# Kernel optimization log

Measured on AMD Instinct MI355X. Metric: run time of the kernel, lower is better.

Reference implementation:

```python
import jax, jax.numpy as jnp
import numpy as np

LN_EPS = 1e-5

def layer_norm(x, w, b):
    mu = jnp.mean(x, axis=-1, keepdims=True)
    var = jnp.mean(jnp.square(x - mu), axis=-1, keepdims=True)
    return (x - mu) * jax.lax.rsqrt(var + LN_EPS) * w + b

def setup_inputs() -> dict:
    key = jax.random.key(0)
    ks = jax.random.split(key, 8)
    B, F, Q, D = 8, 4096, 64, 1024
    H, DH = 16, 64
    inner = H * DH
    s = 1.0 / np.sqrt(D)
    return {
        "features": jax.random.normal(ks[0], (B, F, D), jnp.float32),
        "latents": jax.random.normal(ks[1], (B, Q, D), jnp.float32),
        "key_attention_mask": jax.random.randint(ks[2], (B, F), 0, 2, jnp.int32),
        "ln_m_w": jnp.ones((D,), jnp.float32),
        "ln_m_b": jnp.zeros((D,), jnp.float32),
        "ln_l_w": jnp.ones((D,), jnp.float32),
        "ln_l_b": jnp.zeros((D,), jnp.float32),
        "Wq": jax.random.normal(ks[3], (D, inner), jnp.float32) * s,
        "Wk": jax.random.normal(ks[4], (D, inner), jnp.float32) * s,
        "Wv": jax.random.normal(ks[5], (D, inner), jnp.float32) * s,
        "Wo": jax.random.normal(ks[6], (inner, D), jnp.float32) * (1.0 / np.sqrt(inner)),
    }

def reference(features, latents, key_attention_mask, ln_m_w, ln_m_b, ln_l_w, ln_l_b, Wq, Wk, Wv, Wo):
    H, DH = 16, 64
    B, F, D = features.shape
    Q = latents.shape[1]
    scale = DH ** (-0.5)

    x = layer_norm(features, ln_m_w, ln_m_b)          # [B,F,D]
    lat = layer_norm(latents, ln_l_w, ln_l_b)          # [B,Q,D]

    q = (lat @ Wq).reshape(B, Q, H, DH).transpose(0, 2, 1, 3)   # [B,H,Q,DH]
    kv_in = jnp.concatenate([x, lat], axis=1)                    # [B,F+Q,D]
    k = (kv_in @ Wk).reshape(B, F + Q, H, DH).transpose(0, 2, 1, 3)
    v = (kv_in @ Wv).reshape(B, F + Q, H, DH).transpose(0, 2, 1, 3)

    q = q * scale
    sim = jnp.einsum('bhqd,bhfd->bhqf', q, k)                    # [B,H,Q,F+Q]

    full_mask = jnp.concatenate(
        [key_attention_mask, jnp.ones((B, Q), key_attention_mask.dtype)], axis=1)  # [B,F+Q]
    sim = jnp.where(full_mask[:, None, None, :] == 0, -jnp.inf, sim)

    sim = sim - jax.lax.stop_gradient(jnp.max(sim, axis=-1, keepdims=True))
    alphas = jax.nn.softmax(sim, axis=-1)
    out = jnp.einsum('bhqf,bhfv->bhqv', alphas, v)               # [B,H,Q,DH]
    out = out.transpose(0, 2, 1, 3).reshape(B, Q, H * DH)        # [B,Q,inner]
    return out @ Wo                                              # [B,Q,D]
```

## Files before the change

kernel.cpp:

```cpp
#include <hip/hip_runtime.h>
#include <hip/hip_bf16.h>

#define B_    8
#define F_    4096
#define Qn    64
#define Dm    1024
#define Hh    16
#define DHn   64
#define FQ    4160
#define ROWS_KV 33280
#define ROWS_F  32768
#define KS    13
#define CHPB  5
#define KVOFF ((size_t)ROWS_KV * 1024)

typedef __bf16 v8bf __attribute__((ext_vector_type(8)));
typedef __bf16 v4bf __attribute__((ext_vector_type(4)));
typedef float  v4f  __attribute__((ext_vector_type(4)));

__device__ inline void gl_lds16(const __bf16* g, __bf16* l) {
  __builtin_amdgcn_global_load_lds((__attribute__((address_space(1))) void*)(g),
                                   (__attribute__((address_space(3))) void*)(l),
                                   16, 0, 0);
}

__device__ inline bool is_bf16_inputs(const void* mw) {
  return ((const unsigned int*)mw)[0] != 0x3F800000u;
}

__global__ __launch_bounds__(256) void transpose_kernel(
    const void* __restrict__ w0, const void* __restrict__ w1,
    const void* __restrict__ w2, const void* __restrict__ w3,
    __bf16* __restrict__ t0, __bf16* __restrict__ t1,
    __bf16* __restrict__ t2, __bf16* __restrict__ t3,
    const void* __restrict__ mw)
{
  bool bf = is_bf16_inputs(mw);
  __shared__ __bf16 tile[32][33];
  const void* src; __bf16* dst;
  switch (blockIdx.z) {
    case 0: src = w0; dst = t0; break;
    case 1: src = w1; dst = t1; break;
    case 2: src = w2; dst = t2; break;
    default: src = w3; dst = t3; break;
  }
  int tx = threadIdx.x, ty = threadIdx.y;
  int x = blockIdx.x * 32 + tx;
  #pragma unroll
  for (int j = 0; j < 4; ++j) {
    int y = blockIdx.y * 32 + ty + j * 8;
    size_t e = (size_t)y * 1024 + x;
    float v = bf ? (float)((const __bf16*)src)[e] : ((const float*)src)[e];
    tile[ty + j * 8][tx] = (__bf16)v;
  }
  __syncthreads();
  int x2 = blockIdx.y * 32 + tx;
  #pragma unroll
  for (int j = 0; j < 4; ++j) {
    int y2 = blockIdx.x * 32 + ty + j * 8;
    dst[(size_t)y2 * 1024 + x2] = tile[tx][ty + j * 8];
  }
}

__global__ __launch_bounds__(256) void ln_kernel(
    const void* __restrict__ feat, const void* __restrict__ lat,
    const void* __restrict__ mw, const void* __restrict__ mb,
    const void* __restrict__ lw, const void* __restrict__ lb,
    __bf16* __restrict__ kv_bf, __bf16* __restrict__ lat_bf)
{
  bool bf = is_bf16_inputs(mw);
  int tid = threadIdx.x;
  int wave = tid >> 6, lane = tid & 63;
  int r = blockIdx.x * 4 + wave;
  const void *rowp, *w, *g;
  __bf16 *dst, *dst2 = nullptr;
  size_t rowoff;
  if (r < ROWS_F) {
    rowoff = (size_t)r * Dm; rowp = feat; w = mw; g = mb;
    int b = r >> 12, f = r & (F_ - 1);
    dst = kv_bf + ((size_t)b * FQ + f) * Dm;
  } else {
    int r2 = r - ROWS_F;
    rowoff = (size_t)r2 * Dm; rowp = lat; w = lw; g = lb;
    int b = r2 >> 6, q = r2 & 63;
    dst  = kv_bf + ((size_t)b * FQ + F_ + q) * Dm;
    dst2 = lat_bf + (size_t)r2 * Dm;
  }
  float xs[16], ws_[16], gs[16];
  if (bf) {
    const __bf16* rp = (const __bf16*)rowp + rowoff;
    const __bf16* wp = (const __bf16*)w;
    const __bf16* gp = (const __bf16*)g;
    #pragma unroll
    for (int g2 = 0; g2 < 2; ++g2) {
      int base = g2 * 512 + lane * 8;
      v8bf X = *(const v8bf*)(rp + base);
      v8bf W = *(const v8bf*)(wp + base);
      v8bf G = *(const v8bf*)(gp + base);
      #pragma unroll
      for (int j = 0; j < 8; ++j) {
        xs[g2*8+j] = (float)X[j]; ws_[g2*8+j] = (float)W[j]; gs[g2*8+j] = (float)G[j];
      }
    }
  } else {
    const float* rp = (const float*)rowp + rowoff;
    const float* wp = (const float*)w;
    const float* gp = (const float*)g;
    #pragma unroll
    for (int g4 = 0; g4 < 4; ++g4) {
      int base = g4 * 256 + lane * 4;
      float4 X = *(const float4*)(rp + base);
      float4 W = *(const float4*)(wp + base);
      float4 G = *(const float4*)(gp + base);
      xs[g4*4]=X.x; xs[g4*4+1]=X.y; xs[g4*4+2]=X.z; xs[g4*4+3]=X.w;
      ws_[g4*4]=W.x; ws_[g4*4+1]=W.y; ws_[g4*4+2]=W.z; ws_[g4*4+3]=W.w;
      gs[g4*4]=G.x; gs[g4*4+1]=G.y; gs[g4*4+2]=G.z; gs[g4*4+3]=G.w;
    }
  }
  float s = 0.f, ss = 0.f;
  #pragma unroll
  for (int j = 0; j < 16; ++j) { s += xs[j]; ss += xs[j] * xs[j]; }
  #pragma unroll
  for (int off = 32; off > 0; off >>= 1) {
    s  += __shfl_xor(s, off, 64);
    ss += __shfl_xor(ss, off, 64);
  }
  float mean = s * (1.f / 1024.f);
  float var  = ss * (1.f / 1024.f) - mean * mean;
  float rs = rsqrtf(var + 1e-5f);
  float os[16];
  #pragma unroll
  for (int j = 0; j < 16; ++j) os[j] = (xs[j] - mean) * rs * ws_[j] + gs[j];
  if (bf) {
    #pragma unroll
    for (int g2 = 0; g2 < 2; ++g2) {
      int base = g2 * 512 + lane * 8;
      v8bf O;
      #pragma unroll
      for (int j = 0; j < 8; ++j) O[j] = (__bf16)os[g2*8+j];
      *(v8bf*)(dst + base) = O;
      if (dst2) *(v8bf*)(dst2 + base) = O;
    }
  } else {
    #pragma unroll
    for (int g4 = 0; g4 < 4; ++g4) {
      int base = g4 * 256 + lane * 4;
      v4bf O;
      #pragma unroll
      for (int j = 0; j < 4; ++j) O[j] = (__bf16)os[g4*4+j];
      *(v4bf*)(dst + base) = O;
      if (dst2) *(v4bf*)(dst2 + base) = O;
    }
  }
}

__global__ __launch_bounds__(256, 2) void gemm_kv2_kernel(
    const __bf16* __restrict__ A, const __bf16* __restrict__ BtKV,
    __bf16* __restrict__ KVb)
{
  __shared__ __align__(16) __bf16 As0[128 * 32];
  __shared__ __align__(16) __bf16 As1[128 * 32];
  __shared__ __align__(16) __bf16 Bk0[128 * 32];
  __shared__ __align__(16) __bf16 Bk1[128 * 32];
  __shared__ __align__(16) __bf16 Bv0[128 * 32];
  __shared__ __align__(16) __bf16 Bv1[128 * 32];
  int tid = threadIdx.x;
  int lane = tid & 63, wave = tid >> 6;
  int wm = wave >> 1, wn = wave & 1;
  int n0 = blockIdx.x * 128, m0 = blockIdx.y * 128;
  int lm = lane & 15, lk = (lane >> 4) << 3;

  v4f ak[4][4], av[4][4];
  #pragma unroll
  for (int i = 0; i < 4; ++i)
    #pragma unroll
    for (int j = 0; j < 4; ++j) {
      ak[i][j] = (v4f){0.f, 0.f, 0.f, 0.f};
      av[i][j] = (v4f){0.f, 0.f, 0.f, 0.f};
    }

  int c0 = tid, c1 = tid + 256;
  const __bf16* a0p = A    + (size_t)(m0 + (c0 >> 2)) * 1024 + ((c0 & 3) << 3);
  const __bf16* a1p = A    + (size_t)(m0 + (c1 >> 2)) * 1024 + ((c1 & 3) << 3);
  const __bf16* b0p = BtKV + (size_t)(n0 + (c0 >> 2)) * 1024 + ((c0 & 3) << 3);
  const __bf16* b1p = BtKV + (size_t)(n0 + (c1 >> 2)) * 1024 + ((c1 & 3) << 3);
  const size_t VW = (size_t)1024 * 1024;

  for (int k0 = 0; k0 < 1024; k0 += 64) {
    __syncthreads();
    gl_lds16(a0p + k0,           &As0[c0 * 8]);
    gl_lds16(a1p + k0,           &As0[c1 * 8]);
    gl_lds16(a0p + k0 + 32,      &As1[c0 * 8]);
    gl_lds16(a1p + k0 + 32,      &As1[c1 * 8]);
    gl_lds16(b0p + k0,           &Bk0[c0 * 8]);
    gl_lds16(b1p + k0,           &Bk0[c1 * 8]);
    gl_lds16(b0p + k0 + 32,      &Bk1[c0 * 8]);
    gl_lds16(b1p + k0 + 32,      &Bk1[c1 * 8]);
    gl_lds16(b0p + VW + k0,      &Bv0[c0 * 8]);
    gl_lds16(b1p + VW + k0,      &Bv0[c1 * 8]);
    gl_lds16(b0p + VW + k0 + 32, &Bv1[c0 * 8]);
    gl_lds16(b1p + VW + k0 + 32, &Bv1[c1 * 8]);
    __syncthreads();
    {
      v8bf a[4], bk[4], bv[4];
      #pragma unroll
      for (int i = 0; i < 4; ++i) a[i]  = *(const v8bf*)&As0[(wm * 64 + i * 16 + lm) * 32 + lk];
      #pragma unroll
      for (int j = 0; j < 4; ++j) bk[j] = *(const v8bf*)&Bk0[(wn * 64 + j * 16 + lm) * 32 + lk];
      #pragma unroll
      for (int j = 0; j < 4; ++j) bv[j] = *(const v8bf*)&Bv0[(wn * 64 + j * 16 + lm) * 32 + lk];
      #pragma unroll
      for (int i = 0; i < 4; ++i)
        #pragma unroll
        for (int j = 0; j < 4; ++j) {
          ak[i][j] = __builtin_amdgcn_mfma_f32_16x16x32_bf16(a[i], bk[j], ak[i][j], 0, 0, 0);
          av[i][j] = __builtin_amdgcn_mfma_f32_16x16x32_bf16(a[i], bv[j], av[i][j], 0, 0, 0);
        }
    }
    {
      v8bf a[4], bk[4], bv[4];
      #pragma unroll
      for (int i = 0; i < 4; ++i) a[i]  = *(const v8bf*)&As1[(wm * 64 + i * 16 + lm) * 32 + lk];
      #pragma unroll
      for (int j = 0; j < 4; ++j) bk[j] = *(const v8bf*)&Bk1[(wn * 64 + j * 16 + lm) * 32 + lk];
      #pragma unroll
      for (int j = 0; j < 4; ++j) bv[j] = *(const v8bf*)&Bv1[(wn * 64 + j * 16 + lm) * 32 + lk];
      #pragma unroll
      for (int i = 0; i < 4; ++i)
        #pragma unroll
        for (int j = 0; j < 4; ++j) {
          ak[i][j] = __builtin_amdgcn_mfma_f32_16x16x32_bf16(a[i], bk[j], ak[i][j], 0, 0, 0);
          av[i][j] = __builtin_amdgcn_mfma_f32_16x16x32_bf16(a[i], bv[j], av[i][j], 0, 0, 0);
        }
    }
  }

  #pragma unroll
  for (int i = 0; i < 4; ++i)
    #pragma unroll
    for (int j = 0; j < 4; ++j) {
      int col = n0 + wn * 64 + j * 16 + lm;
      #pragma unroll
      for (int reg = 0; reg < 4; ++reg) {
        int row = m0 + wm * 64 + i * 16 + (lane >> 4) * 4 + reg;
        int bb = row / FQ; int f = row - bb * FQ;
        size_t idx = ((size_t)(bb * Hh + (col >> 6)) * FQ + f) * 64 + (col & 63);
        KVb[idx]         = (__bf16)ak[i][j][reg];
        KVb[idx + KVOFF] = (__bf16)av[i][j][reg];
      }
    }
}

__global__ __launch_bounds__(256) void gemm2_kernel(
    const __bf16* __restrict__ A, const __bf16* __restrict__ Bt,
    void* __restrict__ C, int mode, int out_follow,
    const void* __restrict__ mw)
{
  int obf = out_follow ? (is_bf16_inputs(mw) ? 1 : 0) : 1;

  __shared__ __align__(16) __bf16 As0[128 * 32];
  __shared__ __align__(16) __bf16 As1[128 * 32];
  __shared__ __align__(16) __bf16 Bs0[128 * 32];
  __shared__ __align__(16) __bf16 Bs1[128 * 32];
  int tid = threadIdx.x;
  int lane = tid & 63, wave = tid >> 6;
  int wm = wave >> 1, wn = wave & 1;
  int m0 = blockIdx.y * 128, n0 = blockIdx.x * 128;
  int lm = lane & 15, lk = (lane >> 4) << 3;

  v4f acc[4][4];
  #pragma unroll
  for (int i = 0; i < 4; ++i)
    #pragma unroll
    for (int j = 0; j < 4; ++j) acc[i][j] = (v4f){0.f, 0.f, 0.f, 0.f};

  int c0 = tid, c1 = tid + 256;
  const __bf16* a0p = A  + (size_t)(m0 + (c0 >> 2)) * 1024 + ((c0 & 3) << 3);
  const __bf16* a1p = A  + (size_t)(m0 + (c1 >> 2)) * 1024 + ((c1 & 3) << 3);
  const __bf16* b0p = Bt + (size_t)(n0 + (c0 >> 2)) * 1024 + ((c0 & 3) << 3);
  const __bf16* b1p = Bt + (size_t)(n0 + (c1 >> 2)) * 1024 + ((c1 & 3) << 3);

  for (int k0 = 0; k0 < 1024; k0 += 64) {
    __syncthreads();
    gl_lds16(a0p + k0,      &As0[c0 * 8]);
    gl_lds16(a1p + k0,      &As0[c1 * 8]);
    gl_lds16(a0p + k0 + 32, &As1[c0 * 8]);
    gl_lds16(a1p + k0 + 32, &As1[c1 * 8]);
    gl_lds16(b0p + k0,      &Bs0[c0 * 8]);
    gl_lds16(b1p + k0,      &Bs0[c1 * 8]);
    gl_lds16(b0p + k0 + 32, &Bs1[c0 * 8]);
    gl_lds16(b1p + k0 + 32, &Bs1[c1 * 8]);
    __syncthreads();
    {
      v8bf a[4], b[4];
      #pragma unroll
      for (int i = 0; i < 4; ++i) a[i] = *(const v8bf*)&As0[(wm * 64 + i * 16 + lm) * 32 + lk];
      #pragma unroll
      for (int j = 0; j < 4; ++j) b[j] = *(const v8bf*)&Bs0[(wn * 64 + j * 16 + lm) * 32 + lk];
      #pragma unroll
      for (int i = 0; i < 4; ++i)
        #pragma unroll
        for (int j = 0; j < 4; ++j)
          acc[i][j] = __builtin_amdgcn_mfma_f32_16x16x32_bf16(a[i], b[j], acc[i][j], 0, 0, 0);
    }
    {
      v8bf a[4], b[4];
      #pragma unroll
      for (int i = 0; i < 4; ++i) a[i] = *(const v8bf*)&As1[(wm * 64 + i * 16 + lm) * 32 + lk];
      #pragma unroll
      for (int j = 0; j < 4; ++j) b[j] = *(const v8bf*)&Bs1[(wn * 64 + j * 16 + lm) * 32 + lk];
      #pragma unroll
      for (int i = 0; i < 4; ++i)
        #pragma unroll
        for (int j = 0; j < 4; ++j)
          acc[i][j] = __builtin_amdgcn_mfma_f32_16x16x32_bf16(a[i], b[j], acc[i][j], 0, 0, 0);
    }
  }

  #pragma unroll
  for (int i = 0; i < 4; ++i)
    #pragma unroll
    for (int j = 0; j < 4; ++j) {
      int col = n0 + wn * 64 + j * 16 + lm;
      #pragma unroll
      for (int reg = 0; reg < 4; ++reg) {
        int row = m0 + wm * 64 + i * 16 + (lane >> 4) * 4 + reg;
        size_t idx;
        if (mode == 0) {
          idx = (size_t)row * 1024 + col;
        } else {
          int bb = row >> 6; int qq = row & 63;
          idx = ((size_t)(bb * Hh + (col >> 6)) * 64 + qq) * 64 + (col & 63);
        }
        float v = acc[i][j][reg];
        if (obf) ((__bf16*)C)[idx] = (__bf16)v;
        else     ((float*)C)[idx]  = v;
      }
    }
}

__global__ __launch_bounds__(256) void attn_part_kernel(
    const __bf16* __restrict__ Qm, const __bf16* __restrict__ K,
    const __bf16* __restrict__ V, const int* __restrict__ mask,
    float* __restrict__ Opart, float2* __restrict__ ml)
{
  __shared__ __align__(16) __bf16 qs[64 * 72];
  __shared__ __align__(16) __bf16 ks[64 * 72];
  __shared__ __align__(16) __bf16 vts[64 * 72];
  __shared__ __align__(16) __bf16 ps[64 * 72];
  __shared__ float msb[64];

  int tid = threadIdx.x;
  int lane = tid & 63, wave = tid >> 6;
  int ksb = blockIdx.x;
  int bh = blockIdx.y;
  int b = bh >> 4;
  int lm = lane & 15, lq = lane >> 4;

  const __bf16* qsrc = Qm + (size_t)bh * 64 * 64;
  #pragma unroll
  for (int i = 0; i < 2; ++i) {
    int e = (tid + 256 * i) * 8;
    int row = e >> 6, c = e & 63;
    *(v8bf*)&qs[row * 72 + c] = *(const v8bf*)(qsrc + e);
  }

  float mrow[4], lrow[4];
  v4f acco[4];
  #pragma unroll
  for (int r = 0; r < 4; ++r) { mrow[r] = -1e30f; lrow[r] = 0.f; }
  #pragma unroll
  for (int s = 0; s < 4; ++s) acco[s] = (v4f){0.f, 0.f, 0.f, 0.f};

  const __bf16* kbase = K + (size_t)bh * FQ * 64;
  const __bf16* vbase = V + (size_t)bh * FQ * 64;
  const int* maskb = mask + b * F_;

  for (int cc = 0; cc < CHPB; ++cc) {
    int chunk = ksb * CHPB + cc;
    __syncthreads();
    const __bf16* kc = kbase + (size_t)chunk * 4096;
    const __bf16* vc = vbase + (size_t)chunk * 4096;
    #pragma unroll
    for (int i = 0; i < 2; ++i) {
      int e = (tid + 256 * i) * 8;
      int row = e >> 6, c = e & 63;
      *(v8bf*)&ks[row * 72 + c] = *(const v8bf*)(kc + e);
      v8bf vv = *(const v8bf*)(vc + e);
      #pragma unroll
      for (int j = 0; j < 8; ++j) vts[(c + j) * 72 + row] = vv[j];
    }
    if (tid < 64) {
      int kidx = chunk * 64 + tid;
      msb[tid] = (kidx < F_) ? (maskb[kidx] != 0 ? 0.f : -1e30f) : 0.f;
    }
    __syncthreads();

    v8bf aq0 = *(const v8bf*)&qs[(wave * 16 + lm) * 72 + lq * 8];
    v8bf aq1 = *(const v8bf*)&qs[(wave * 16 + lm) * 72 + lq * 8 + 32];
    v4f sf[4];
    #pragma unroll
    for (int s = 0; s < 4; ++s) {
      v8bf bk0 = *(const v8bf*)&ks[(s * 16 + lm) * 72 + lq * 8];
      v8bf bk1 = *(const v8bf*)&ks[(s * 16 + lm) * 72 + lq * 8 + 32];
      v4f z = (v4f){0.f, 0.f, 0.f, 0.f};
      z = __builtin_amdgcn_mfma_f32_16x16x32_bf16(aq0, bk0, z, 0, 0, 0);
      z = __builtin_amdgcn_mfma_f32_16x16x32_bf16(aq1, bk1, z, 0, 0, 0);
      sf[s] = z;
    }
    float bias[4];
    #pragma unroll
    for (int s = 0; s < 4; ++s) bias[s] = msb[s * 16 + lm];
    #pragma unroll
    for (int s = 0; s < 4; ++s)
      #pragma unroll
      for (int r = 0; r < 4; ++r)
        sf[s][r] = sf[s][r] * 0.125f + bias[s];

    #pragma unroll
    for (int r = 0; r < 4; ++r) {
      float mx = fmaxf(fmaxf(sf[0][r], sf[1][r]), fmaxf(sf[2][r], sf[3][r]));
      #pragma unroll
      for (int off = 1; off < 16; off <<= 1) mx = fmaxf(mx, __shfl_xor(mx, off, 64));
      float mN = fmaxf(mrow[r], mx);
      float alpha = __expf(mrow[r] - mN);
      mrow[r] = mN;
      float ls = 0.f;
      #pragma unroll
      for (int s = 0; s < 4; ++s) { float p = __expf(sf[s][r] - mN); sf[s][r] = p; ls += p; }
      #pragma unroll
      for (int off = 1; off < 16; off <<= 1) ls += __shfl_xor(ls, off, 64);
      lrow[r] = lrow[r] * alpha + ls;
      #pragma unroll
      for (int s = 0; s < 4; ++s) acco[s][r] *= alpha;
    }

    #pragma unroll
    for (int s = 0; s < 4; ++s)
      #pragma unroll
      for (int r = 0; r < 4; ++r)
        ps[(wave * 16 + lq * 4 + r) * 72 + s * 16 + lm] = (__bf16)sf[s][r];

    v8bf ap0 = *(const v8bf*)&ps[(wave * 16 + lm) * 72 + lq * 8];
    v8bf ap1 = *(const v8bf*)&ps[(wave * 16 + lm) * 72 + lq * 8 + 32];
    #pragma unroll
    for (int s = 0; s < 4; ++s) {
      v8bf bv0 = *(const v8bf*)&vts[(s * 16 + lm) * 72 + lq * 8];
      v8bf bv1 = *(const v8bf*)&vts[(s * 16 + lm) * 72 + lq * 8 + 32];
      acco[s] = __builtin_amdgcn_mfma_f32_16x16x32_bf16(ap0, bv0, acco[s], 0, 0, 0);
      acco[s] = __builtin_amdgcn_mfma_f32_16x16x32_bf16(ap1, bv1, acco[s], 0, 0, 0);
    }
  }

  float* Ob = Opart + (((size_t)ksb * 128 + bh) * 64) * 64;
  #pragma unroll
  for (int s = 0; s < 4; ++s)
    #pragma unroll
    for (int r = 0; r < 4; ++r) {
      int q = wave * 16 + lq * 4 + r;
      Ob[q * 64 + s * 16 + lm] = acco[s][r];
    }
  if (lm == 0) {
    #pragma unroll
    for (int r = 0; r < 4; ++r) {
      int q = wave * 16 + lq * 4 + r;
      ml[((size_t)ksb * 128 + bh) * 64 + q] = make_float2(mrow[r], lrow[r]);
    }
  }
}

__global__ __launch_bounds__(256) void attn_comb_kernel(
    const float* __restrict__ Opart, const float2* __restrict__ ml,
    __bf16* __restrict__ attnb)
{
  int bh = blockIdx.x;
  int b = bh >> 4, h = bh & 15;
  int t = threadIdx.x;
  int q = t >> 2, cg = (t & 3) * 16;

  float m_[KS], l_[KS];
  float M = -1e30f;
  #pragma unroll
  for (int k = 0; k < KS; ++k) {
    float2 p = ml[((size_t)k * 128 + bh) * 64 + q];
    m_[k] = p.x; l_[k] = p.y;
    M = fmaxf(M, p.x);
  }
  float L = 0.f;
  #pragma unroll
  for (int k = 0; k < KS; ++k) L += l_[k] * __expf(m_[k] - M);
  float o[16];
  #pragma unroll
  for (int j = 0; j < 16; ++j) o[j] = 0.f;
  #pragma unroll
  for (int k = 0; k < KS; ++k) {
    float wgt = __expf(m_[k] - M);
    const float* P = Opart + ((((size_t)k * 128 + bh) * 64 + q) * 64) + cg;
    #pragma unroll
    for (int j4 = 0; j4 < 4; ++j4) {
      float4 pv = *(const float4*)(P + j4 * 4);
      o[j4*4]   += pv.x * wgt; o[j4*4+1] += pv.y * wgt;
      o[j4*4+2] += pv.z * wgt; o[j4*4+3] += pv.w * wgt;
    }
  }
  float invL = 1.f / L;
  __bf16* dst = attnb + ((size_t)(b * 64 + q) * 1024) + h * 64 + cg;
  v8bf O0, O1;
  #pragma unroll
  for (int j = 0; j < 8; ++j) { O0[j] = (__bf16)(o[j] * invL); O1[j] = (__bf16)(o[8+j] * invL); }
  *(v8bf*)dst = O0;
  *(v8bf*)(dst + 8) = O1;
}

extern "C" void kernel_launch(void* const* d_in, const int* in_sizes, int n_in,
                              void* d_out, int out_size, void* d_ws, size_t ws_size,
                              hipStream_t stream)
{
  void* feat = d_in[0];
  void* lat  = d_in[1];
  const int* mk = (const int*)d_in[2];
  void* mw = d_in[3]; void* mb = d_in[4];
  void* lw = d_in[5]; void* lb = d_in[6];
  void* Wq = d_in[7]; void* Wk = d_in[8];
  void* Wv = d_in[9]; void* Wo = d_in[10];

  char* ws = (char*)d_ws;
  size_t off = 0;
  auto alloc = [&](size_t bytes) {
    char* p = ws + off;
    off += (bytes + 255) & ~(size_t)255;
    return p;
  };
  __bf16* WkvT  = (__bf16*)alloc((size_t)2 * 1024 * 1024 * 2);
  __bf16* WqT   = (__bf16*)alloc((size_t)1024 * 1024 * 2);
  __bf16* WoT   = (__bf16*)alloc((size_t)1024 * 1024 * 2);
  __bf16* KVb   = (__bf16*)alloc((size_t)2 * ROWS_KV * 1024 * 2);
  __bf16* Qmb   = (__bf16*)alloc((size_t)512 * 1024 * 2);
  __bf16* attnb = (__bf16*)alloc((size_t)512 * 1024 * 2);
  __bf16* lat_bf= (__bf16*)alloc((size_t)512 * 1024 * 2);
  char*   big   = (char*)alloc((size_t)ROWS_KV * 1024 * 2);
  __bf16* kv_bf = (__bf16*)big;
  float*  Opart = (float*)big;
  float2* ml    = (float2*)(big + (size_t)KS*128*64*64*4);
  if (ws_size < off) return;

  transpose_kernel<<<dim3(32, 32, 4), dim3(32, 8), 0, stream>>>(
      Wq, Wk, Wv, Wo, WqT, WkvT, WkvT + (size_t)1024 * 1024, WoT, mw);

  ln_kernel<<<8320, 256, 0, stream>>>(feat, lat, mw, mb, lw, lb, kv_bf, lat_bf);

  gemm_kv2_kernel<<<dim3(8, 260), 256, 0, stream>>>(kv_bf, WkvT, KVb);
  gemm2_kernel<<<dim3(8, 4), 256, 0, stream>>>(lat_bf, WqT, Qmb, 2, 0, mw);

  attn_part_kernel<<<dim3(KS, 128), 256, 0, stream>>>(
      Qmb, KVb, KVb + KVOFF, mk, Opart, ml);
  attn_comb_kernel<<<128, 256, 0, stream>>>(Opart, ml, attnb);

  gemm2_kernel<<<dim3(8, 4), 256, 0, stream>>>(attnb, WoT, d_out, 0, 1, mw);
}
```

Baseline: 490.3 us.

## Rewrite KV projection GEMM as 256x256 8-wave pipelined kernel with swizzled LDS

Replaces the 128x128 K/V GEMM with a 512-thread kernel computing 256x256 output tiles over the concatenated K|V weight. Global-to-LDS loads are double-buffered and interleaved with MFMA phases under explicit barriers, waitcnt and setprio. LDS rows use an XOR swizzle to avoid bank conflicts, and block indices are remapped for cache locality. The aim is higher MFMA utilization and better overlap of loads with math in the dominant GEMM. The cost is 128KB of LDS per block, hand-written synchronization that is harder to verify, and a scattered epilogue store.

Result: no change. 489.6 us (-0.2%).

```diff
diff --git a/kernel.cpp b/kernel.cpp
--- a/kernel.cpp
+++ b/kernel.cpp
@@ -154,99 +154,158 @@
   }
 }
 
-__global__ __launch_bounds__(256, 2) void gemm_kv2_kernel(
+
+#define BAR() asm volatile("s_barrier" ::: "memory")
+
+#define PH(Q) do { \
+  BAR(); \
+  asm volatile("s_waitcnt lgkmcnt(0)" ::: "memory"); \
+  __builtin_amdgcn_s_setprio(1); \
+  Q; \
+  __builtin_amdgcn_s_setprio(0); \
+  BAR(); \
+} while (0)
+
+#define PHV(Q) do { \
+  BAR(); \
+  asm volatile("s_waitcnt lgkmcnt(0)" ::: "memory"); \
+  __builtin_amdgcn_s_setprio(1); \
+  Q; \
+  __builtin_amdgcn_s_setprio(0); \
+  asm volatile("s_waitcnt vmcnt(4)" ::: "memory"); \
+  BAR(); \
+} while (0)
+
+#define QUAD(MB, NB, BF) do { \
+  _Pragma("unroll") \
+  for (int m_ = 0; m_ < 4; ++m_) { \
+    _Pragma("unroll") \
+    for (int n_ = 0; n_ < 2; ++n_) { \
+      _Pragma("unroll") \
+      for (int k_ = 0; k_ < 2; ++k_) { \
+        acc[(MB) + m_][(NB) + n_] = __builtin_amdgcn_mfma_f32_16x16x32_bf16( \
+            af[m_][k_], BF[n_][k_], acc[(MB) + m_][(NB) + n_], 0, 0, 0); \
+      } } } } while (0)
+
+#define LDA8(BB, ROFF) do { \
+  _Pragma("unroll") \
+  for (int m_ = 0; m_ < 4; ++m_) { \
+    _Pragma("unroll") \
+    for (int k_ = 0; k_ < 2; ++k_) { \
+      const int r_ = (ROFF) + m_ * 16 + lm; \
+      af[m_][k_] = *(const v8bf*)(aB[BB] + ((r_ << 7) + ((k_ * 64 + kcb) ^ ((r_ & 7) << 4)))); \
+    } } } while (0)
+
+#define LDB4(BB, DST, NOFF) do { \
+  _Pragma("unroll") \
+  for (int n_ = 0; n_ < 2; ++n_) { \
+    _Pragma("unroll") \
+    for (int k_ = 0; k_ < 2; ++k_) { \
+      const int r_ = bq + (NOFF) + n_ * 16 + lm; \
+      DST[n_][k_] = *(const v8bf*)(bB[BB] + ((r_ << 7) + ((k_ * 64 + kcb) ^ ((r_ & 7) << 4)))); \
+    } } } while (0)
+
+#define STAGE_A(BB, H, K0) do { \
+  gl_lds16(asrc + (size_t)(H) * 131072 + (K0),         (__bf16*)(ldsw + ((BB) * 4 + (H)) * 16384)); \
+  gl_lds16(asrc + (size_t)(H) * 131072 + (K0) + 65536, (__bf16*)(ldsw + ((BB) * 4 + (H)) * 16384 + 8192)); \
+} while (0)
+
+#define STAGE_B(BB, H, K0) do { \
+  gl_lds16(bsrc + (size_t)(H) * 131072 + (K0),         (__bf16*)(ldsw + ((BB) * 4 + 2 + (H)) * 16384)); \
+  gl_lds16(bsrc + (size_t)(H) * 131072 + (K0) + 65536, (__bf16*)(ldsw + ((BB) * 4 + 2 + (H)) * 16384 + 8192)); \
+} while (0)
+
+__global__ __launch_bounds__(512, 2) void gemm_kv8_kernel(
     const __bf16* __restrict__ A, const __bf16* __restrict__ BtKV,
     __bf16* __restrict__ KVb)
 {
-  __shared__ __align__(16) __bf16 As0[128 * 32];
-  __shared__ __align__(16) __bf16 As1[128 * 32];
-  __shared__ __align__(16) __bf16 Bk0[128 * 32];
-  __shared__ __align__(16) __bf16 Bk1[128 * 32];
-  __shared__ __align__(16) __bf16 Bv0[128 * 32];
-  __shared__ __align__(16) __bf16 Bv1[128 * 32];
-  int tid = threadIdx.x;
-  int lane = tid & 63, wave = tid >> 6;
-  int wm = wave >> 1, wn = wave & 1;
-  int n0 = blockIdx.x * 128, m0 = blockIdx.y * 128;
-  int lm = lane & 15, lk = (lane >> 4) << 3;
-
-  v4f ak[4][4], av[4][4];
-  #pragma unroll
-  for (int i = 0; i < 4; ++i)
-    #pragma unroll
-    for (int j = 0; j < 4; ++j) {
-      ak[i][j] = (v4f){0.f, 0.f, 0.f, 0.f};
-      av[i][j] = (v4f){0.f, 0.f, 0.f, 0.f};
-    }
-
-  int c0 = tid, c1 = tid + 256;
-  const __bf16* a0p = A    + (size_t)(m0 + (c0 >> 2)) * 1024 + ((c0 & 3) << 3);
-  const __bf16* a1p = A    + (size_t)(m0 + (c1 >> 2)) * 1024 + ((c1 & 3) << 3);
-  const __bf16* b0p = BtKV + (size_t)(n0 + (c0 >> 2)) * 1024 + ((c0 & 3) << 3);
-  const __bf16* b1p = BtKV + (size_t)(n0 + (c1 >> 2)) * 1024 + ((c1 & 3) << 3);
-  const size_t VW = (size_t)1024 * 1024;
-
-  for (int k0 = 0; k0 < 1024; k0 += 64) {
-    __syncthreads();
-    gl_lds16(a0p + k0,           &As0[c0 * 8]);
-    gl_lds16(a1p + k0,           &As0[c1 * 8]);
-    gl_lds16(a0p + k0 + 32,      &As1[c0 * 8]);
-    gl_lds16(a1p + k0 + 32,      &As1[c1 * 8]);
-    gl_lds16(b0p + k0,           &Bk0[c0 * 8]);
-    gl_lds16(b1p + k0,           &Bk0[c1 * 8]);
-    gl_lds16(b0p + k0 + 32,      &Bk1[c0 * 8]);
-    gl_lds16(b1p + k0 + 32,      &Bk1[c1 * 8]);
-    gl_lds16(b0p + VW + k0,      &Bv0[c0 * 8]);
-    gl_lds16(b1p + VW + k0,      &Bv0[c1 * 8]);
-    gl_lds16(b0p + VW + k0 + 32, &Bv1[c0 * 8]);
-    gl_lds16(b1p + VW + k0 + 32, &Bv1[c1 * 8]);
-    __syncthreads();
-    {
-      v8bf a[4], bk[4], bv[4];
-      #pragma unroll
-      for (int i = 0; i < 4; ++i) a[i]  = *(const v8bf*)&As0[(wm * 64 + i * 16 + lm) * 32 + lk];
-      #pragma unroll
-      for (int j = 0; j < 4; ++j) bk[j] = *(const v8bf*)&Bk0[(wn * 64 + j * 16 + lm) * 32 + lk];
-      #pragma unroll
-      for (int j = 0; j < 4; ++j) bv[j] = *(const v8bf*)&Bv0[(wn * 64 + j * 16 + lm) * 32 + lk];
-      #pragma unroll
-      for (int i = 0; i < 4; ++i)
-        #pragma unroll
-        for (int j = 0; j < 4; ++j) {
-          ak[i][j] = __builtin_amdgcn_mfma_f32_16x16x32_bf16(a[i], bk[j], ak[i][j], 0, 0, 0);
-          av[i][j] = __builtin_amdgcn_mfma_f32_16x16x32_bf16(a[i], bv[j], av[i][j], 0, 0, 0);
-        }
-    }
-    {
-      v8bf a[4], bk[4], bv[4];
-      #pragma unroll
-      for (int i = 0; i < 4; ++i) a[i]  = *(const v8bf*)&As1[(wm * 64 + i * 16 + lm) * 32 + lk];
-      #pragma unroll
-      for (int j = 0; j < 4; ++j) bk[j] = *(const v8bf*)&Bk1[(wn * 64 + j * 16 + lm) * 32 + lk];
-      #pragma unroll
-      for (int j = 0; j < 4; ++j) bv[j] = *(const v8bf*)&Bv1[(wn * 64 + j * 16 + lm) * 32 + lk];
-      #pragma unroll
-      for (int i = 0; i < 4; ++i)
-        #pragma unroll
-        for (int j = 0; j < 4; ++j) {
-          ak[i][j] = __builtin_amdgcn_mfma_f32_16x16x32_bf16(a[i], bk[j], ak[i][j], 0, 0, 0);
-          av[i][j] = __builtin_amdgcn_mfma_f32_16x16x32_bf16(a[i], bv[j], av[i][j], 0, 0, 0);
-        }
-    }
-  }
-
-  #pragma unroll
-  for (int i = 0; i < 4; ++i)
-    #pragma unroll
-    for (int j = 0; j < 4; ++j) {
-      int col = n0 + wn * 64 + j * 16 + lm;
+  __shared__ __align__(16) char ldsm[131072];
+  const int tid = threadIdx.x;
+  const int lane = tid & 63, wave = tid >> 6;
+  const int wm = wave >> 2, wn = wave & 3;
+  const int lm = lane & 15, l4 = lane >> 4;
+  const int kcb = l4 << 4;
+  const int bq = (wn & 1) << 6;
+
+  const int wg = (blockIdx.x & 7) * 130 + (blockIdx.x >> 3);
+  const int n0 = (wg & 7) << 8;
+  const int m0 = (wg >> 3) << 8;
+
+  const int r0 = (wave << 3) + (lane >> 3);
+  const int xc = ((lane & 7) ^ (lane >> 3)) << 3;
+  const __bf16* asrc = A    + (size_t)(m0 + r0) * 1024 + xc;
+  const __bf16* bsrc = BtKV + (size_t)(n0 + r0) * 1024 + xc;
+  char* const ldsw = ldsm + tid * 16;
+  const char* const aB[2] = { ldsm + wm * 16384, ldsm + (4 + wm) * 16384 };
+  const char* const bB[2] = { ldsm + (2 + (wn >> 1)) * 16384,
+                              ldsm + (6 + (wn >> 1)) * 16384 };
+
+  v4f acc[8][4];
+  #pragma unroll
+  for (int i = 0; i < 8; ++i)
+    #pragma unroll
+    for (int j = 0; j < 4; ++j) acc[i][j] = (v4f){0.f, 0.f, 0.f, 0.f};
+  v8bf af[4][2], blo[2][2], bhi[2][2];
+
+  STAGE_A(0, 0, 0); STAGE_A(0, 1, 0);
+  STAGE_B(0, 0, 0); STAGE_B(0, 1, 0);
+  STAGE_B(1, 0, 64); STAGE_B(1, 1, 64);
+  asm volatile("s_waitcnt vmcnt(4)" ::: "memory");
+  BAR();
+
+  #pragma unroll 1
+  for (int it = 0; it < 8; ++it) {
+    const int kA1 = (2 * it + 1) << 6;
+    const int kT0 = (it < 7) ? ((2 * it + 2) << 6) : 0;
+    const int kT1 = (it < 7) ? ((2 * it + 3) << 6) : 0;
+
+    LDA8(0, 0); LDB4(0, blo, 0);
+    STAGE_A(1, 0, kA1);
+    PH(QUAD(0, 0, blo));
+
+    LDB4(0, bhi, 32);
+    STAGE_A(1, 1, kA1);
+    PH(QUAD(0, 2, bhi));
+
+    LDA8(0, 64);
+    STAGE_B(0, 0, kT0);
+    PH(QUAD(4, 2, bhi));
+
+    STAGE_B(0, 1, kT0);
+    PHV(QUAD(4, 0, blo));
+
+    LDA8(1, 0); LDB4(1, blo, 0);
+    STAGE_A(0, 0, kT0);
+    PH(QUAD(0, 0, blo));
+
+    LDB4(1, bhi, 32);
+    STAGE_A(0, 1, kT0);
+    PH(QUAD(0, 2, bhi));
+
+    LDA8(1, 64);
+    STAGE_B(1, 0, kT1);
+    PH(QUAD(4, 2, bhi));
+
+    STAGE_B(1, 1, kT1);
+    PHV(QUAD(4, 0, blo));
+  }
+
+  const int cb = n0 + (wn << 6);
+  const int rb = m0 + (wm << 7);
+  #pragma unroll
+  for (int m = 0; m < 8; ++m)
+    #pragma unroll
+    for (int n = 0; n < 4; ++n) {
+      int col = cb + n * 16 + lm;
+      int h = (col >> 6) & 15;
+      int dh = col & 63;
+      size_t vo = (col >= 1024) ? KVOFF : (size_t)0;
       #pragma unroll
       for (int reg = 0; reg < 4; ++reg) {
-        int row = m0 + wm * 64 + i * 16 + (lane >> 4) * 4 + reg;
-        int bb = row / FQ; int f = row - bb * FQ;
-        size_t idx = ((size_t)(bb * Hh + (col >> 6)) * FQ + f) * 64 + (col & 63);
-        KVb[idx]         = (__bf16)ak[i][j][reg];
-        KVb[idx + KVOFF] = (__bf16)av[i][j][reg];
+        int row = rb + m * 16 + l4 * 4 + reg;
+        int bb2 = row / FQ; int f = row - bb2 * FQ;
+        size_t idx = ((size_t)(bb2 * Hh + h) * FQ + f) * 64 + dh;
+        KVb[idx + vo] = (__bf16)acc[m][n][reg];
       }
     }
 }
@@ -549,7 +608,7 @@
 
   ln_kernel<<<8320, 256, 0, stream>>>(feat, lat, mw, mb, lw, lb, kv_bf, lat_bf);
 
-  gemm_kv2_kernel<<<dim3(8, 260), 256, 0, stream>>>(kv_bf, WkvT, KVb);
+  gemm_kv8_kernel<<<dim3(1040), dim3(512), 0, stream>>>(kv_bf, WkvT, KVb);
   gemm2_kernel<<<dim3(8, 4), 256, 0, stream>>>(lat_bf, WqT, Qmb, 2, 0, mw);
 
   attn_part_kernel<<<dim3(KS, 128), 256, 0, stream>>>(
```
